# Optimization experiments

Hardware: AMD Instinct MI355X
Metric: run time of the kernel (lower is better)

## Reference

```python
import jax, jax.numpy as jnp
import numpy as np

# Static problem sizes (must be static for segment ops under jit)
N = 2048   # num nodes (seq_len)
M = 50     # num hyperedges (hyper_num); original uses max(edge_id)+1, guaranteed hit with 8192 draws
C = 64     # out_channels (= in_channels here)
BT = 64    # batch
E = 8192   # incidences = k(=4) hyperedges per node
NEG_SLOPE = 0.2
MARGIN = 4.2


def setup_inputs() -> dict:
    key = jax.random.key(0)
    k1, k2, k3, k4, k5 = jax.random.split(key, 5)
    x = jax.random.normal(k1, (BT, N, C), jnp.float32)
    weight = jax.random.normal(k2, (C, C), jnp.float32) * (1.0 / np.sqrt(C))  # glorot-ish
    att = jax.random.normal(k3, (1, 1, 2 * C), jnp.float32) * 0.1
    node_idx = jax.random.randint(k4, (E,), 0, N, dtype=jnp.int32)
    edge_idx = jax.random.randint(k5, (E,), 0, M, dtype=jnp.int32)
    return {"x": x, "weight": weight, "att": att, "node_idx": node_idx, "edge_idx": edge_idx}


def _safe_norm(v, axis):
    # norm with zero (not NaN/inf) gradient at 0, matching torch.norm subgradient
    sq = jnp.sum(v * v, axis=axis)
    pos = sq > 0
    return jnp.where(pos, jnp.sqrt(jnp.where(pos, sq, 1.0)), 0.0)


def _segment_softmax(logits, seg, num_segments):
    # grouped softmax over incidences sharing the same node id (PyG softmax)
    mx = jax.ops.segment_max(logits, seg, num_segments=num_segments)
    mx = jnp.where(jnp.isfinite(mx), mx, 0.0)  # empty segments
    e = jnp.exp(logits - mx[seg])
    s = jax.ops.segment_sum(e, seg, num_segments=num_segments)
    return e / (s[seg] + 1e-16)


def reference(x, weight, att, node_idx, edge_idx):
    xw = jnp.einsum('bnc,cd->bnd', x, weight)          # [B,N,C] dense GEMM
    x1 = jnp.transpose(xw, (1, 0, 2))                  # [N,B,C]
    x_i = x1[node_idx]                                 # [E,B,C] gather per incidence
    edge_sums = jax.ops.segment_sum(x_i, edge_idx, num_segments=M)  # [M,B,C] per-edge aggregate
    x_j = edge_sums[edge_idx]                          # [E,B,C]

    # pairwise hyperedge contrastive loss (vectorized double loop over edges)
    inner = jnp.einsum('kbc,mbc->kmb', edge_sums, edge_sums)  # [M,M,B]
    nrm = _safe_norm(edge_sums, axis=-1)               # [M,B]
    cos = inner / (nrm[:, None, :] * nrm[None, :, :])
    diff = edge_sums[:, None] - edge_sums[None, :]     # [M,M,B,C]
    dist = _safe_norm(diff, axis=-1)                   # [M,M,B]
    loss_item = cos * dist + (1.0 - cos) * jnp.maximum(MARGIN - dist, 0.0)
    loss_hyper = jnp.sum(jnp.abs(jnp.mean(loss_item, axis=-1))) / float((M + 1) ** 2)

    # per-incidence attention, softmax grouped by node
    logits = jnp.sum(jnp.concatenate([x_i, x_j], axis=-1) * att.reshape(1, 1, 2 * C), axis=-1)  # [E,B]
    logits = jax.nn.leaky_relu(logits, NEG_SLOPE)
    alpha = _segment_softmax(logits, node_idx, N)      # [E,B] (dropout skipped: eval mode)

    ones = jnp.ones((E,), xw.dtype)
    D = jax.ops.segment_sum(ones, node_idx, num_segments=N)    # node degree
    Bdeg = jax.ops.segment_sum(ones, edge_idx, num_segments=M) # hyperedge degree
    Bnorm = jnp.where(Bdeg > 0, 1.0 / Bdeg, 0.0)

    # propagate pass 1: nodes -> hyperedges (source_to_target)
    msg1 = Bnorm[edge_idx][:, None, None] * alpha[:, :, None] * x_i
    edge_feat = jax.ops.segment_sum(msg1, edge_idx, num_segments=M)  # [M,B,C]
    # propagate pass 2: hyperedges -> nodes (target_to_source)
    msg2 = D[node_idx][:, None, None] * alpha[:, :, None] * edge_feat[edge_idx]
    out = jax.ops.segment_sum(msg2, node_idx, num_segments=N)        # [N,B,C]
    out = jnp.transpose(out, (1, 0, 2))               # [B,N,C]

    constrain_losstotal = jnp.abs(jnp.mean(x_i - x_j)) + loss_hyper
    return out, constrain_losstotal
```

## Files before the change

kernel.cpp:

```cpp
#include <hip/hip_runtime.h>
#include <math.h>

#define NN 2048
#define MM 50
#define CC 64
#define BB 64
#define EE 8192
#define NEG 0.2f
#define MARGIN_ 4.2f
#define ETILE 320
#define NPAIRBLK 625
#define NSEG (NN+MM)

__global__ __launch_bounds__(256) void k_bg(
    const float* __restrict__ x, const float* __restrict__ w, const float* __restrict__ att,
    const int* __restrict__ nidx, const int* __restrict__ eidx,
    float* __restrict__ outf, float* __restrict__ natt1, float* __restrict__ rsBN,
    int* __restrict__ ncnt, int* __restrict__ noff, int* __restrict__ ecnt,
    int* __restrict__ eoff, int* __restrict__ nlist, int* __restrict__ elist){
  __shared__ float Xl[64*68];
  __shared__ float Wl[64*64];
  __shared__ int wcnt[4], wlt[4];
  int t = threadIdx.x;
  int bid = blockIdx.x;

  if (bid < NSEG){
    int seg = bid;
    const int* key; int target; int* outl;
    if (seg < NN){ key=nidx; target=seg;    outl=nlist; }
    else         { key=eidx; target=seg-NN; outl=elist; }
    int wv=t>>6, lane=t&63;
    int q0 = wv*2048;
    int cm=0, cl=0;
    for (int i=lane; i<2048; i+=64){
      int k = key[q0+i];
      cm += (k==target); cl += (k<target);
    }
    #pragma unroll
    for (int m=32;m>=1;m>>=1){ cm += __shfl_xor(cm,m,64); cl += __shfl_xor(cl,m,64); }
    if (lane==0){ wcnt[wv]=cm; wlt[wv]=cl; }
    __syncthreads();
    int base = wlt[0]+wlt[1]+wlt[2]+wlt[3];
    int wstart = base;
    for (int i=0;i<wv;++i) wstart += wcnt[i];
    unsigned long long ltmask = (1ull<<lane) - 1ull;
    int carry = 0;
    for (int wq=0; wq<32; ++wq){
      int e = q0 + wq*64 + lane;
      bool mm = (key[e]==target);
      unsigned long long bal = __ballot(mm);
      if (mm) outl[wstart + carry + __popcll(bal & ltmask)] = e;
      carry += __popcll(bal);
    }
    if (t==0){
      int tot = wcnt[0]+wcnt[1]+wcnt[2]+wcnt[3];
      if (seg<NN){ ncnt[seg]=tot; noff[seg]=base; }
      else       { ecnt[seg-NN]=tot; eoff[seg-NN]=base; }
    }
    return;
  }

  size_t rbase = (size_t)(bid - NSEG)*64;
  {
    const float4* xs = (const float4*)(x + rbase*CC);
    const float4* wsrc = (const float4*)w;
    #pragma unroll
    for (int i=0;i<4;++i){
      int idx = t + i*256;
      int r = idx>>4, c4 = idx&15;
      float4 v = xs[idx];
      *(float4*)&Xl[r*68 + c4*4] = v;
      ((float4*)Wl)[idx] = wsrc[idx];
    }
  }
  __syncthreads();
  int rg = t>>4, cg = t&15;
  int c0 = cg*4;
  float acc[4][4];
  #pragma unroll
  for (int i=0;i<4;++i){ acc[i][0]=0.f; acc[i][1]=0.f; acc[i][2]=0.f; acc[i][3]=0.f; }
  #pragma unroll
  for (int ks=0; ks<16; ++ks){
    int k0 = ks*4;
    float4 Wf0 = *(const float4*)&Wl[(k0+0)*64 + c0];
    float4 Wf1 = *(const float4*)&Wl[(k0+1)*64 + c0];
    float4 Wf2 = *(const float4*)&Wl[(k0+2)*64 + c0];
    float4 Wf3 = *(const float4*)&Wl[(k0+3)*64 + c0];
    #pragma unroll
    for (int ri=0;ri<4;++ri){
      float4 Xf = *(const float4*)&Xl[(rg*4+ri)*68 + k0];
      acc[ri][0] += Xf.x*Wf0.x; acc[ri][1] += Xf.x*Wf0.y; acc[ri][2] += Xf.x*Wf0.z; acc[ri][3] += Xf.x*Wf0.w;
      acc[ri][0] += Xf.y*Wf1.x; acc[ri][1] += Xf.y*Wf1.y; acc[ri][2] += Xf.y*Wf1.z; acc[ri][3] += Xf.y*Wf1.w;
      acc[ri][0] += Xf.z*Wf2.x; acc[ri][1] += Xf.z*Wf2.y; acc[ri][2] += Xf.z*Wf2.z; acc[ri][3] += Xf.z*Wf2.w;
      acc[ri][0] += Xf.w*Wf3.x; acc[ri][1] += Xf.w*Wf3.y; acc[ri][2] += Xf.w*Wf3.z; acc[ri][3] += Xf.w*Wf3.w;
    }
  }
  #pragma unroll
  for (int ri=0;ri<4;++ri){
    size_t row = rbase + rg*4 + ri;
    *(float4*)&outf[row*CC + c0] = make_float4(acc[ri][0],acc[ri][1],acc[ri][2],acc[ri][3]);
  }
  float4 at1 = *(const float4*)(att + c0);
  #pragma unroll
  for (int ri=0;ri<4;++ri){
    float a1 = acc[ri][0]*at1.x + acc[ri][1]*at1.y + acc[ri][2]*at1.z + acc[ri][3]*at1.w;
    float rs = (acc[ri][0]+acc[ri][1]) + (acc[ri][2]+acc[ri][3]);
    #pragma unroll
    for (int m=8;m>=1;m>>=1){
      a1 += __shfl_xor(a1,m,64);
      rs += __shfl_xor(rs,m,64);
    }
    if (cg==0){
      size_t row = rbase + rg*4 + ri;
      int b = (int)(row>>11), n = (int)(row&(NN-1));
      natt1[n*BB+b]=a1; rsBN[row]=rs;
    }
  }
}

__global__ __launch_bounds__(256) void k_es(
    const int* __restrict__ elist,const int* __restrict__ eoff,
    const int* __restrict__ ecnt,const int* __restrict__ nidx,
    const float* __restrict__ outf,const float* __restrict__ att,
    float* __restrict__ es,float* __restrict__ nrm,float* __restrict__ eatt2,
    float* __restrict__ gpart3,
    const float* __restrict__ rsBN,const int* __restrict__ ncnt,
    float* __restrict__ gpart2){
  __shared__ int lds_n[ETILE];
  __shared__ float red2[256];
  int bid = blockIdx.x, t = threadIdx.x;

  if (bid >= MM*4){
    int k = bid - MM*4;
    float s = 0.f;
    for (int i=k*256+t; i<NN*BB; i+=32*256) s += rsBN[i]*(float)ncnt[i&(NN-1)];
    red2[t]=s; __syncthreads();
    for (int st=128;st>0;st>>=1){ if(t<st) red2[t]+=red2[t+st]; __syncthreads(); }
    if (t==0) gpart2[k]=red2[0];
    return;
  }

  int m = bid>>2, bq = bid&3;
  int bi = t>>4;
  int b  = bq*16 + bi;
  int c0 = (t&15)*4;
  int off = eoff[m], deg = ecnt[m];
  float4 as=make_float4(0.f,0.f,0.f,0.f);
  for (int tb=0; tb<deg; tb+=ETILE){
    int tl = min(ETILE, deg-tb);
    __syncthreads();
    for (int j=t;j<tl;j+=256) lds_n[j]=nidx[elist[off+tb+j]];
    __syncthreads();
    #pragma unroll 4
    for (int j=0;j<tl;++j){
      int n = lds_n[j];
      float4 v = *(const float4*)&outf[(size_t)b*(NN*CC) + (size_t)n*CC + c0];
      as.x+=v.x; as.y+=v.y; as.z+=v.z; as.w+=v.w;
    }
  }
  size_t o = ((size_t)m*BB+b)*CC+c0;
  *(float4*)&es[o]=as;
  float ssq = as.x*as.x+as.y*as.y+as.z*as.z+as.w*as.w;
  float4 at2 = *(const float4*)(att + CC + c0);
  float ea = as.x*at2.x+as.y*at2.y+as.z*at2.z+as.w*at2.w;
  #pragma unroll
  for (int s=8;s>=1;s>>=1){ ssq += __shfl_xor(ssq,s,64); ea += __shfl_xor(ea,s,64); }
  if ((t&15)==0){
    nrm[m*BB+b] = ssq>0.f? sqrtf(ssq):0.f;
    eatt2[m*BB+b] = ea;
  }
  red2[t] = (as.x+as.y)+(as.z+as.w);
  __syncthreads();
  for (int s=128;s>0;s>>=1){ if(t<s) red2[t]+=red2[t+s]; __syncthreads(); }
  if (t==0) gpart3[bid] = red2[0]*(float)deg;
}

__global__ __launch_bounds__(256) void k_ap(
    const float* __restrict__ es,const float* __restrict__ nrm,
    float* __restrict__ pairl,
    const int* __restrict__ nlist,const int* __restrict__ noff,
    const int* __restrict__ ncnt,const int* __restrict__ eidx,
    const float* __restrict__ natt1,const float* __restrict__ eatt2,
    float* __restrict__ alpha){
  int bid = blockIdx.x, t = threadIdx.x;
  int wv = t>>6, b = t&63;

  if (bid < NPAIRBLK){
    int km = bid*4 + wv;
    if (km >= MM*MM) return;
    int kk = km / MM, m = km % MM;
    const float4* pa = (const float4*)&es[((size_t)kk*BB+b)*CC];
    const float4* pb = (const float4*)&es[((size_t)m*BB+b)*CC];
    float inner=0.f, d2=0.f;
    #pragma unroll
    for (int q=0;q<16;++q){
      float4 a=pa[q], c=pb[q];
      inner += a.x*c.x+a.y*c.y+a.z*c.z+a.w*c.w;
      float dx=a.x-c.x, dy=a.y-c.y, dz=a.z-c.z, dw=a.w-c.w;
      d2 += dx*dx+dy*dy+dz*dz+dw*dw;
    }
    float dist = d2>0.f? sqrtf(d2):0.f;
    float cosv = inner/(nrm[kk*BB+b]*nrm[m*BB+b]);
    float li = cosv*dist + (1.f-cosv)*fmaxf(MARGIN_-dist,0.f);
    #pragma unroll
    for (int s=32;s>=1;s>>=1) li += __shfl_xor(li,s,64);
    if (b==0) pairl[km] = fabsf(li*(1.f/64.f));
    return;
  }

  int n = (bid - NPAIRBLK)*4 + wv;
  if (n >= NN) return;
  int off = noff[n], deg = ncnt[n];
  if (deg==0) return;
  float na = natt1[n*BB+b];
  float mx = -1e30f;
  for (int j=0;j<deg;++j){
    int e = nlist[off+j]; int m = eidx[e];
    float l = na + eatt2[m*BB+b]; l = l>0.f? l : NEG*l;
    mx = fmaxf(mx,l);
  }
  float s=0.f;
  for (int j=0;j<deg;++j){
    int e = nlist[off+j]; int m = eidx[e];
    float l = na + eatt2[m*BB+b]; l = l>0.f? l : NEG*l;
    s += expf(l-mx);
  }
  float inv = 1.f/(s+1e-16f);
  for (int j=0;j<deg;++j){
    int e = nlist[off+j]; int m = eidx[e];
    float l = na + eatt2[m*BB+b]; l = l>0.f? l : NEG*l;
    alpha[(size_t)e*BB+b] = expf(l-mx)*inv;
  }
}

__global__ __launch_bounds__(256) void k_ef(
    const int* __restrict__ elist,const int* __restrict__ eoff,
    const int* __restrict__ ecnt,const int* __restrict__ nidx,
    const float* __restrict__ outf,const float* __restrict__ alpha,
    float* __restrict__ ef){
  __shared__ int   lds_e[ETILE];
  __shared__ int   lds_n[ETILE];
  __shared__ float lds_al[ETILE*16];
  int m = blockIdx.x>>2, bq = blockIdx.x&3;
  int t = threadIdx.x;
  int bi = t>>4;
  int b  = bq*16 + bi;
  int c0 = (t&15)*4;
  int off = eoff[m], deg = ecnt[m];
  float4 af=make_float4(0.f,0.f,0.f,0.f);
  for (int tb=0; tb<deg; tb+=ETILE){
    int tl = min(ETILE, deg-tb);
    __syncthreads();
    for (int j=t;j<tl;j+=256){
      int e = elist[off+tb+j];
      lds_e[j]=e; lds_n[j]=nidx[e];
    }
    __syncthreads();
    for (int idx=t; idx<tl*16; idx+=256){
      int j=idx>>4, b2=idx&15;
      lds_al[idx] = alpha[(size_t)lds_e[j]*BB + bq*16 + b2];
    }
    __syncthreads();
    #pragma unroll 4
    for (int j=0;j<tl;++j){
      int n = lds_n[j];
      float al = lds_al[j*16+bi];
      float4 v = *(const float4*)&outf[(size_t)b*(NN*CC) + (size_t)n*CC + c0];
      af.x+=al*v.x; af.y+=al*v.y; af.z+=al*v.z; af.w+=al*v.w;
    }
  }
  float bn = deg>0 ? 1.f/(float)deg : 0.f;
  size_t o = ((size_t)m*BB+b)*CC+c0;
  float4 f; f.x=af.x*bn; f.y=af.y*bn; f.z=af.z*bn; f.w=af.w*bn;
  *(float4*)&ef[o]=f;
}

__global__ __launch_bounds__(256) void k_outl(
    const int* __restrict__ nlist,const int* __restrict__ noff,
    const int* __restrict__ ncnt,const int* __restrict__ eidx,
    const float* __restrict__ alpha,const float* __restrict__ ef,
    const float* __restrict__ pairl,const float* __restrict__ gpart2,
    const float* __restrict__ gpart3,
    float* __restrict__ outf){
  __shared__ float r1[256],r2[256],r3[256];
  int bid = blockIdx.x, t = threadIdx.x;

  if (bid == NN){
    float s1=0.f,s2=0.f,s3=0.f;
    for (int i=t;i<MM*MM;i+=256) s1+=pairl[i];
    if (t<32) s2=gpart2[t];
    for (int i=t;i<MM*4;i+=256) s3+=gpart3[i];
    r1[t]=s1;r2[t]=s2;r3[t]=s3; __syncthreads();
    for (int s=128;s>0;s>>=1){ if(t<s){r1[t]+=r1[t+s];r2[t]+=r2[t+s];r3[t]+=r3[t+s];} __syncthreads(); }
    if (t==0){
      float lh = r1[0]/2601.f;
      float con = fabsf((r2[0]-r3[0])*(1.f/33554432.f));
      outf[(size_t)NN*BB*CC] = con+lh;
    }
    return;
  }

  int n = bid;
  int b = t>>2, sub = t&3;
  int off = noff[n], deg = ncnt[n];
  float4 a0=make_float4(0.f,0.f,0.f,0.f),a1=a0,a2=a0,a3=a0;
  for (int j=0;j<deg;++j){
    int e = nlist[off+j]; int m = eidx[e];
    float al = alpha[(size_t)e*BB+b];
    const float4* p = (const float4*)&ef[((size_t)m*BB+b)*CC + sub*16];
    float4 v0=p[0],v1=p[1],v2=p[2],v3=p[3];
    a0.x+=al*v0.x; a0.y+=al*v0.y; a0.z+=al*v0.z; a0.w+=al*v0.w;
    a1.x+=al*v1.x; a1.y+=al*v1.y; a1.z+=al*v1.z; a1.w+=al*v1.w;
    a2.x+=al*v2.x; a2.y+=al*v2.y; a2.z+=al*v2.z; a2.w+=al*v2.w;
    a3.x+=al*v3.x; a3.y+=al*v3.y; a3.z+=al*v3.z; a3.w+=al*v3.w;
  }
  float D=(float)deg;
  float* o = &outf[(size_t)b*(NN*CC) + (size_t)n*CC + sub*16];
  ((float4*)o)[0]=make_float4(D*a0.x,D*a0.y,D*a0.z,D*a0.w);
  ((float4*)o)[1]=make_float4(D*a1.x,D*a1.y,D*a1.z,D*a1.w);
  ((float4*)o)[2]=make_float4(D*a2.x,D*a2.y,D*a2.z,D*a2.w);
  ((float4*)o)[3]=make_float4(D*a3.x,D*a3.y,D*a3.z,D*a3.w);
}

extern "C" void kernel_launch(void* const* d_in, const int* in_sizes, int n_in,
                              void* d_out, int out_size, void* d_ws, size_t ws_size,
                              hipStream_t stream){
  (void)in_sizes; (void)n_in; (void)out_size; (void)ws_size;
  const float* x    = (const float*)d_in[0];
  const float* w    = (const float*)d_in[1];
  const float* att  = (const float*)d_in[2];
  const int*   nidx = (const int*)d_in[3];
  const int*   eidx = (const int*)d_in[4];
  float* outf = (float*)d_out;

  char* ws = (char*)d_ws;
  size_t off = 0;
  auto alloc = [&](size_t bytes)->void*{ void* p = ws + off; off = (off + bytes + 255) & ~(size_t)255; return p; };
  float* natt1 = (float*)alloc(sizeof(float)*NN*BB);
  float* eatt2 = (float*)alloc(sizeof(float)*MM*BB);
  float* alpha = (float*)alloc(sizeof(float)*(size_t)EE*BB);
  float* es    = (float*)alloc(sizeof(float)*MM*BB*CC);
  float* ef    = (float*)alloc(sizeof(float)*MM*BB*CC);
  float* nrm   = (float*)alloc(sizeof(float)*MM*BB);
  float* pairl = (float*)alloc(sizeof(float)*MM*MM);
  float* rsBN  = (float*)alloc(sizeof(float)*NN*BB);
  float* gpart2= (float*)alloc(sizeof(float)*32);
  float* gpart3= (float*)alloc(sizeof(float)*MM*4);
  int* ncnt = (int*)alloc(sizeof(int)*NN);
  int* noff = (int*)alloc(sizeof(int)*NN);
  int* ecnt = (int*)alloc(sizeof(int)*MM);
  int* eoff = (int*)alloc(sizeof(int)*MM);
  int* nlist= (int*)alloc(sizeof(int)*EE);
  int* elist= (int*)alloc(sizeof(int)*EE);

  k_bg  <<<NSEG + (NN*BB)/64, 256, 0, stream>>>(x, w, att, nidx, eidx,
                                                outf, natt1, rsBN,
                                                ncnt, noff, ecnt, eoff, nlist, elist);
  k_es  <<<MM*4 + 32, 256, 0, stream>>>(elist, eoff, ecnt, nidx, outf, att,
                                        es, nrm, eatt2, gpart3, rsBN, ncnt, gpart2);
  k_ap  <<<NPAIRBLK + NN/4, 256, 0, stream>>>(es, nrm, pairl,
                                              nlist, noff, ncnt, eidx, natt1, eatt2, alpha);
  k_ef  <<<MM*4, 256, 0, stream>>>(elist, eoff, ecnt, nidx, outf, alpha, ef);
  k_outl<<<NN + 1, 256, 0, stream>>>(nlist, noff, ncnt, eidx, alpha, ef,
                                     pairl, gpart2, gpart3, outf);
}
```

Baseline: 128.2 us.

## Defer weight GEMM past gathers using linearity and fold att into weights

```diff
diff --git a/kernel.cpp b/kernel.cpp
--- a/kernel.cpp
+++ b/kernel.cpp
@@ -15,12 +15,11 @@
 __global__ __launch_bounds__(256) void k_bg(
     const float* __restrict__ x, const float* __restrict__ w, const float* __restrict__ att,
     const int* __restrict__ nidx, const int* __restrict__ eidx,
-    float* __restrict__ outf, float* __restrict__ natt1, float* __restrict__ rsBN,
+    float* __restrict__ natt1, float* __restrict__ rsBN,
     int* __restrict__ ncnt, int* __restrict__ noff, int* __restrict__ ecnt,
     int* __restrict__ eoff, int* __restrict__ nlist, int* __restrict__ elist){
-  __shared__ float Xl[64*68];
-  __shared__ float Wl[64*64];
   __shared__ int wcnt[4], wlt[4];
+  __shared__ float wa[64], wo[64];
   int t = threadIdx.x;
   int bid = blockIdx.x;
 
@@ -60,74 +59,52 @@
     return;
   }
 
+  if (t < 64){
+    float sa=0.f, so=0.f;
+    const float4* wr = (const float4*)(w + t*CC);
+    #pragma unroll
+    for (int i=0;i<16;++i){
+      float4 wv = wr[i];
+      float4 a1 = *(const float4*)(att + i*4);
+      sa += wv.x*a1.x + wv.y*a1.y + wv.z*a1.z + wv.w*a1.w;
+      so += (wv.x+wv.y)+(wv.z+wv.w);
+    }
+    wa[t]=sa; wo[t]=so;
+  }
+  __syncthreads();
   size_t rbase = (size_t)(bid - NSEG)*64;
-  {
-    const float4* xs = (const float4*)(x + rbase*CC);
-    const float4* wsrc = (const float4*)w;
-    #pragma unroll
-    for (int i=0;i<4;++i){
-      int idx = t + i*256;
-      int r = idx>>4, c4 = idx&15;
-      float4 v = xs[idx];
-      *(float4*)&Xl[r*68 + c4*4] = v;
-      ((float4*)Wl)[idx] = wsrc[idx];
-    }
-  }
-  __syncthreads();
-  int rg = t>>4, cg = t&15;
-  int c0 = cg*4;
-  float acc[4][4];
+  int r = t>>2, q = t&3;
+  size_t row = rbase + r;
+  const float4* xr = (const float4*)(x + row*CC);
+  float s1=0.f, s2=0.f;
   #pragma unroll
-  for (int i=0;i<4;++i){ acc[i][0]=0.f; acc[i][1]=0.f; acc[i][2]=0.f; acc[i][3]=0.f; }
+  for (int i=0;i<4;++i){
+    float4 xv = xr[q*4+i];
+    float4 av = *(const float4*)&wa[q*16+i*4];
+    float4 ov = *(const float4*)&wo[q*16+i*4];
+    s1 += xv.x*av.x + xv.y*av.y + xv.z*av.z + xv.w*av.w;
+    s2 += xv.x*ov.x + xv.y*ov.y + xv.z*ov.z + xv.w*ov.w;
+  }
   #pragma unroll
-  for (int ks=0; ks<16; ++ks){
-    int k0 = ks*4;
-    float4 Wf0 = *(const float4*)&Wl[(k0+0)*64 + c0];
-    float4 Wf1 = *(const float4*)&Wl[(k0+1)*64 + c0];
-    float4 Wf2 = *(const float4*)&Wl[(k0+2)*64 + c0];
-    float4 Wf3 = *(const float4*)&Wl[(k0+3)*64 + c0];
-    #pragma unroll
-    for (int ri=0;ri<4;++ri){
-      float4 Xf = *(const float4*)&Xl[(rg*4+ri)*68 + k0];
-      acc[ri][0] += Xf.x*Wf0.x; acc[ri][1] += Xf.x*Wf0.y; acc[ri][2] += Xf.x*Wf0.z; acc[ri][3] += Xf.x*Wf0.w;
-      acc[ri][0] += Xf.y*Wf1.x; acc[ri][1] += Xf.y*Wf1.y; acc[ri][2] += Xf.y*Wf1.z; acc[ri][3] += Xf.y*Wf1.w;
-      acc[ri][0] += Xf.z*Wf2.x; acc[ri][1] += Xf.z*Wf2.y; acc[ri][2] += Xf.z*Wf2.z; acc[ri][3] += Xf.z*Wf2.w;
-      acc[ri][0] += Xf.w*Wf3.x; acc[ri][1] += Xf.w*Wf3.y; acc[ri][2] += Xf.w*Wf3.z; acc[ri][3] += Xf.w*Wf3.w;
-    }
-  }
-  #pragma unroll
-  for (int ri=0;ri<4;++ri){
-    size_t row = rbase + rg*4 + ri;
-    *(float4*)&outf[row*CC + c0] = make_float4(acc[ri][0],acc[ri][1],acc[ri][2],acc[ri][3]);
-  }
-  float4 at1 = *(const float4*)(att + c0);
-  #pragma unroll
-  for (int ri=0;ri<4;++ri){
-    float a1 = acc[ri][0]*at1.x + acc[ri][1]*at1.y + acc[ri][2]*at1.z + acc[ri][3]*at1.w;
-    float rs = (acc[ri][0]+acc[ri][1]) + (acc[ri][2]+acc[ri][3]);
-    #pragma unroll
-    for (int m=8;m>=1;m>>=1){
-      a1 += __shfl_xor(a1,m,64);
-      rs += __shfl_xor(rs,m,64);
-    }
-    if (cg==0){
-      size_t row = rbase + rg*4 + ri;
-      int b = (int)(row>>11), n = (int)(row&(NN-1));
-      natt1[n*BB+b]=a1; rsBN[row]=rs;
-    }
+  for (int m=1;m<=2;m<<=1){ s1 += __shfl_xor(s1,m,64); s2 += __shfl_xor(s2,m,64); }
+  if (q==0){
+    int b = (int)(row>>11), n = (int)(row&(NN-1));
+    natt1[n*BB+b]=s1; rsBN[row]=s2;
   }
 }
 
 __global__ __launch_bounds__(256) void k_es(
     const int* __restrict__ elist,const int* __restrict__ eoff,
     const int* __restrict__ ecnt,const int* __restrict__ nidx,
-    const float* __restrict__ outf,const float* __restrict__ att,
+    const float* __restrict__ x,const float* __restrict__ w,const float* __restrict__ att,
     float* __restrict__ es,float* __restrict__ nrm,float* __restrict__ eatt2,
     float* __restrict__ gpart3,
     const float* __restrict__ rsBN,const int* __restrict__ ncnt,
     float* __restrict__ gpart2){
   __shared__ int lds_n[ETILE];
   __shared__ float red2[256];
+  __shared__ float Wl[4096];
+  __shared__ float xsl[16*68];
   int bid = blockIdx.x, t = threadIdx.x;
 
   if (bid >= MM*4){
@@ -145,6 +122,11 @@
   int b  = bq*16 + bi;
   int c0 = (t&15)*4;
   int off = eoff[m], deg = ecnt[m];
+  {
+    const float4* wsrc = (const float4*)w;
+    #pragma unroll
+    for (int i=0;i<4;++i) ((float4*)Wl)[t + i*256] = wsrc[t + i*256];
+  }
   float4 as=make_float4(0.f,0.f,0.f,0.f);
   for (int tb=0; tb<deg; tb+=ETILE){
     int tl = min(ETILE, deg-tb);
@@ -154,22 +136,32 @@
     #pragma unroll 4
     for (int j=0;j<tl;++j){
       int n = lds_n[j];
-      float4 v = *(const float4*)&outf[(size_t)b*(NN*CC) + (size_t)n*CC + c0];
+      float4 v = *(const float4*)&x[((size_t)b*NN + n)*CC + c0];
       as.x+=v.x; as.y+=v.y; as.z+=v.z; as.w+=v.w;
     }
   }
+  __syncthreads();
+  *(float4*)&xsl[bi*68 + c0] = as;
+  __syncthreads();
+  float4 e4 = make_float4(0.f,0.f,0.f,0.f);
+  #pragma unroll 8
+  for (int k=0;k<64;++k){
+    float xv = xsl[bi*68 + k];
+    float4 wv = *(const float4*)&Wl[k*64 + c0];
+    e4.x += xv*wv.x; e4.y += xv*wv.y; e4.z += xv*wv.z; e4.w += xv*wv.w;
+  }
   size_t o = ((size_t)m*BB+b)*CC+c0;
-  *(float4*)&es[o]=as;
-  float ssq = as.x*as.x+as.y*as.y+as.z*as.z+as.w*as.w;
+  *(float4*)&es[o]=e4;
+  float ssq = e4.x*e4.x+e4.y*e4.y+e4.z*e4.z+e4.w*e4.w;
   float4 at2 = *(const float4*)(att + CC + c0);
-  float ea = as.x*at2.x+as.y*at2.y+as.z*at2.z+as.w*at2.w;
+  float ea = e4.x*at2.x+e4.y*at2.y+e4.z*at2.z+e4.w*at2.w;
   #pragma unroll
   for (int s=8;s>=1;s>>=1){ ssq += __shfl_xor(ssq,s,64); ea += __shfl_xor(ea,s,64); }
   if ((t&15)==0){
     nrm[m*BB+b] = ssq>0.f? sqrtf(ssq):0.f;
     eatt2[m*BB+b] = ea;
   }
-  red2[t] = (as.x+as.y)+(as.z+as.w);
+  red2[t] = (e4.x+e4.y)+(e4.z+e4.w);
   __syncthreads();
   for (int s=128;s>0;s>>=1){ if(t<s) red2[t]+=red2[t+s]; __syncthreads(); }
   if (t==0) gpart3[bid] = red2[0]*(float)deg;
@@ -236,17 +228,25 @@
 __global__ __launch_bounds__(256) void k_ef(
     const int* __restrict__ elist,const int* __restrict__ eoff,
     const int* __restrict__ ecnt,const int* __restrict__ nidx,
-    const float* __restrict__ outf,const float* __restrict__ alpha,
+    const float* __restrict__ x,const float* __restrict__ w,
+    const float* __restrict__ alpha,
     float* __restrict__ ef){
   __shared__ int   lds_e[ETILE];
   __shared__ int   lds_n[ETILE];
   __shared__ float lds_al[ETILE*16];
+  __shared__ float Wl[4096];
+  __shared__ float xsl[16*68];
   int m = blockIdx.x>>2, bq = blockIdx.x&3;
   int t = threadIdx.x;
   int bi = t>>4;
   int b  = bq*16 + bi;
   int c0 = (t&15)*4;
   int off = eoff[m], deg = ecnt[m];
+  {
+    const float4* wsrc = (const float4*)w;
+    #pragma unroll
+    for (int i=0;i<4;++i) ((float4*)Wl)[t + i*256] = wsrc[t + i*256];
+  }
   float4 af=make_float4(0.f,0.f,0.f,0.f);
   for (int tb=0; tb<deg; tb+=ETILE){
     int tl = min(ETILE, deg-tb);
@@ -265,13 +265,23 @@
     for (int j=0;j<tl;++j){
       int n = lds_n[j];
       float al = lds_al[j*16+bi];
-      float4 v = *(const float4*)&outf[(size_t)b*(NN*CC) + (size_t)n*CC + c0];
+      float4 v = *(const float4*)&x[((size_t)b*NN + n)*CC + c0];
       af.x+=al*v.x; af.y+=al*v.y; af.z+=al*v.z; af.w+=al*v.w;
     }
+  }
+  __syncthreads();
+  *(float4*)&xsl[bi*68 + c0] = af;
+  __syncthreads();
+  float4 e4 = make_float4(0.f,0.f,0.f,0.f);
+  #pragma unroll 8
+  for (int k=0;k<64;++k){
+    float xv = xsl[bi*68 + k];
+    float4 wv = *(const float4*)&Wl[k*64 + c0];
+    e4.x += xv*wv.x; e4.y += xv*wv.y; e4.z += xv*wv.z; e4.w += xv*wv.w;
   }
   float bn = deg>0 ? 1.f/(float)deg : 0.f;
   size_t o = ((size_t)m*BB+b)*CC+c0;
-  float4 f; f.x=af.x*bn; f.y=af.y*bn; f.z=af.z*bn; f.w=af.w*bn;
+  float4 f; f.x=e4.x*bn; f.y=e4.y*bn; f.z=e4.z*bn; f.w=e4.w*bn;
   *(float4*)&ef[o]=f;
 }
 
@@ -354,13 +364,13 @@
   int* elist= (int*)alloc(sizeof(int)*EE);
 
   k_bg  <<<NSEG + (NN*BB)/64, 256, 0, stream>>>(x, w, att, nidx, eidx,
-                                                outf, natt1, rsBN,
+                                                natt1, rsBN,
                                                 ncnt, noff, ecnt, eoff, nlist, elist);
-  k_es  <<<MM*4 + 32, 256, 0, stream>>>(elist, eoff, ecnt, nidx, outf, att,
+  k_es  <<<MM*4 + 32, 256, 0, stream>>>(elist, eoff, ecnt, nidx, x, w, att,
                                         es, nrm, eatt2, gpart3, rsBN, ncnt, gpart2);
   k_ap  <<<NPAIRBLK + NN/4, 256, 0, stream>>>(es, nrm, pairl,
                                               nlist, noff, ncnt, eidx, natt1, eatt2, alpha);
-  k_ef  <<<MM*4, 256, 0, stream>>>(elist, eoff, ecnt, nidx, outf, alpha, ef);
+  k_ef  <<<MM*4, 256, 0, stream>>>(elist, eoff, ecnt, nidx, x, w, alpha, ef);
   k_outl<<<NN + 1, 256, 0, stream>>>(nlist, noff, ncnt, eidx, alpha, ef,
                                      pairl, gpart2, gpart3, outf);
 }
```

After: 120.2 us. -6.2%, faster.
